# Performance work log

Measured on AMD Instinct MI355X. Metric: run time of the kernel, lower is better.

Reference implementation:

```python
import jax, jax.numpy as jnp
import numpy as np

N_NODES = 100000
N_EDGES = 3200000
D_FEAT = 256
GC_HID = 20      # CVAEEncoder.hidden_dim default
DEC_HID = 40     # CVAEDecoder.hidden_dim default
Z_DIM = 32
EXPR_DIM = 256
SIGMA_BOUND = 0.0001


def setup_inputs() -> dict:
    key = jax.random.key(0)
    ks = jax.random.split(key, 16)
    inp = {
        "nodes": jax.random.normal(ks[0], (N_NODES, D_FEAT), dtype=jnp.float32),
        "senders": jax.random.randint(ks[1], (N_EDGES,), 0, N_NODES, dtype=jnp.int32),
        "receivers": jax.random.randint(ks[2], (N_EDGES,), 0, N_NODES, dtype=jnp.int32),
        "eps": jax.random.normal(ks[3], (N_NODES, Z_DIM), dtype=jnp.float32),
    }
    def dense(k, fan_in, fan_out):
        # flax default: lecun_normal kernel, zero bias
        w = jax.random.normal(k, (fan_in, fan_out), dtype=jnp.float32) / np.sqrt(fan_in)
        return w, jnp.zeros((fan_out,), jnp.float32)
    inp["W_gc1"], inp["b_gc1"] = dense(ks[4], D_FEAT, GC_HID)
    inp["W_gc2"], inp["b_gc2"] = dense(ks[5], GC_HID, GC_HID)
    inp["W_mu"], inp["b_mu"] = dense(ks[6], GC_HID + D_FEAT, Z_DIM)
    inp["W_ls"], inp["b_ls"] = dense(ks[7], GC_HID + D_FEAT, Z_DIM)
    inp["W_d1"], inp["b_d1"] = dense(ks[8], Z_DIM, DEC_HID)
    inp["W_d2"], inp["b_d2"] = dense(ks[9], DEC_HID, EXPR_DIM)
    return inp


def _gcn_layer(h, senders, receivers, W, b):
    # jraph.GraphConvolution: update_node_fn = softmax(relu(Dense(x))),
    # then symmetric-normalized segment_sum aggregation (no self edges).
    h = jax.nn.softmax(jax.nn.relu(h @ W + b), axis=-1)  # [N, GC_HID]
    ones = jnp.ones(senders.shape, h.dtype)
    deg_s = jax.ops.segment_sum(ones, senders, N_NODES)
    deg_r = jax.ops.segment_sum(ones, receivers, N_NODES)
    h = h * jax.lax.rsqrt(jnp.maximum(deg_s, 1.0))[:, None]
    h = jax.ops.segment_sum(h[senders], receivers, N_NODES)  # irregular gather+scatter
    h = h * jax.lax.rsqrt(jnp.maximum(deg_r, 1.0))[:, None]
    return h


def reference(nodes, senders, receivers, eps,
              W_gc1, b_gc1, W_gc2, b_gc2,
              W_mu, b_mu, W_ls, b_ls,
              W_d1, b_d1, W_d2, b_d2):
    # Encoder: 2 GC layers
    h = _gcn_layer(nodes, senders, receivers, W_gc1, b_gc1)
    h = _gcn_layer(h, senders, receivers, W_gc2, b_gc2)
    h = jnp.concatenate([h, nodes], axis=-1)  # [N, GC_HID + D_FEAT]
    mu = h @ W_mu + b_mu
    logsig2 = h @ W_ls + b_ls
    # Reparameterization
    sigma = SIGMA_BOUND + jnp.exp(0.5 * logsig2)
    z = mu + sigma * eps
    # Decoder MLP (nlayers=2 -> one hidden relu layer)
    d = jax.nn.relu(z @ W_d1 + b_d1)
    Xsample = d @ W_d2 + b_d2
    return Xsample, mu, logsig2
```

## Files before the change

### kernel.cpp

```cpp
#include <hip/hip_runtime.h>
#include <math.h>

#define N_NODES 100000
#define N_EDGES 3200000
#define D_FEAT 256
#define GC_HID 20
#define DEC_HID 40
#define Z_DIM 32

#define EPB 2048
#define NBLK 1563
#define SB 392
#define SBSH 8
#define S2CAP 12288


__device__ inline unsigned short f2bf(float f) {
    unsigned u = __float_as_uint(f);
    return (unsigned short)((u + 0x7FFFu + ((u >> 16) & 1u)) >> 16);
}
__device__ inline float bf2f(unsigned short h) {
    return __uint_as_float((unsigned)h << 16);
}

__global__ __launch_bounds__(96) void k_wpack(const float* __restrict__ W1,
                                              const float* __restrict__ Wmu,
                                              const float* __restrict__ Wls,
                                              float* __restrict__ Wp) {
    int k = blockIdx.x, j = threadIdx.x;
    float v = 0.0f;
    if (j < 20) v = W1[k * GC_HID + j];
    else if (j >= 24 && j < 56) v = Wmu[(GC_HID + k) * Z_DIM + (j - 24)];
    else if (j >= 56 && j < 88) v = Wls[(GC_HID + k) * Z_DIM + (j - 56)];
    Wp[k * 96 + j] = v;
}

__global__ __launch_bounds__(512) void k_sort(const int* __restrict__ snd,
                                              const int* __restrict__ rcv,
                                              unsigned* __restrict__ rec_r,
                                              unsigned char* __restrict__ rec_s,
                                              unsigned short* __restrict__ srow_r,
                                              unsigned short* __restrict__ srow_s) {
    __shared__ int es[EPB], er[EPB];
    __shared__ unsigned scan[SB + 1];
    __shared__ unsigned cur[SB];
    __shared__ unsigned sorted[EPB];
    __shared__ unsigned char sorteds[EPB];
    int b = blockIdx.x, t = threadIdx.x;
    int base = b * EPB;
    int cnt = min(EPB, N_EDGES - base);
    for (int i = t; i < cnt; i += 512) { es[i] = snd[base + i]; er[i] = rcv[base + i]; }

    for (int i = t; i < SB + 1; i += 512) scan[i] = 0u;
    __syncthreads();
    for (int i = t; i < cnt; i += 512) atomicAdd(&scan[(er[i] >> SBSH) + 1], 1u);
    __syncthreads();
    for (int off = 1; off < SB + 1; off <<= 1) {
        unsigned v = (t >= off && t < SB + 1) ? scan[t - off] : 0u;
        __syncthreads();
        if (t < SB + 1) scan[t] += v;
        __syncthreads();
    }
    for (int i = t; i < SB + 1; i += 512) srow_r[(size_t)b * (SB + 1) + i] = (unsigned short)scan[i];
    if (t < SB) cur[t] = scan[t];
    __syncthreads();
    for (int i = t; i < cnt; i += 512) {
        int r = er[i];
        unsigned pos = atomicAdd(&cur[r >> SBSH], 1u);
        sorted[pos] = ((unsigned)(r & 255) << 17) | (unsigned)es[i];
    }
    __syncthreads();
    for (int i = t; i < cnt; i += 512) rec_r[(size_t)base + i] = sorted[i];
    __syncthreads();

    for (int i = t; i < SB + 1; i += 512) scan[i] = 0u;
    __syncthreads();
    for (int i = t; i < cnt; i += 512) atomicAdd(&scan[(es[i] >> SBSH) + 1], 1u);
    __syncthreads();
    for (int off = 1; off < SB + 1; off <<= 1) {
        unsigned v = (t >= off && t < SB + 1) ? scan[t - off] : 0u;
        __syncthreads();
        if (t < SB + 1) scan[t] += v;
        __syncthreads();
    }
    for (int i = t; i < SB + 1; i += 512) srow_s[(size_t)b * (SB + 1) + i] = (unsigned short)scan[i];
    if (t < SB) cur[t] = scan[t];
    __syncthreads();
    for (int i = t; i < cnt; i += 512) {
        int s = es[i];
        unsigned pos = atomicAdd(&cur[s >> SBSH], 1u);
        sorteds[pos] = (unsigned char)(s & 255);
    }
    __syncthreads();
    for (int i = t; i < cnt; i += 512) rec_s[(size_t)base + i] = sorteds[i];
}

__global__ __launch_bounds__(512) void k_degs(const unsigned char* __restrict__ rec_s,
                                              const unsigned short* __restrict__ srow_s,
                                              float* __restrict__ rs_s) {
    __shared__ unsigned h[256];
    int s = blockIdx.x, t = threadIdx.x;
    if (t < 256) h[t] = 0u;
    __syncthreads();
    for (int k = t; k < NBLK; k += 512) {
        const unsigned short* row = srow_s + (size_t)k * (SB + 1);
        unsigned st = row[s], en = row[s + 1];
        const unsigned char* rp = rec_s + (size_t)k * EPB;
        for (unsigned i = st; i < en; ++i) atomicAdd(&h[rp[i]], 1u);
    }
    __syncthreads();
    if (t < 256) {
        int n = (s << SBSH) + t;
        if (n < N_NODES) rs_s[n] = rsqrtf(fmaxf((float)h[t], 1.0f));
    }
}

__global__ __launch_bounds__(256) void k_scanB(const unsigned short* __restrict__ srow_r,
                                               unsigned* __restrict__ pref_t,
                                               unsigned* __restrict__ gtot) {
    __shared__ unsigned buf[256];
    int s = blockIdx.x, t = threadIdx.x;
    unsigned run = 0;
    for (int k0 = 0; k0 < NBLK; k0 += 256) {
        int k = k0 + t;
        unsigned v = 0;
        if (k < NBLK) {
            const unsigned short* row = srow_r + (size_t)k * (SB + 1);
            v = (unsigned)row[s + 1] - (unsigned)row[s];
        }
        buf[t] = v;
        __syncthreads();
        for (int off = 1; off < 256; off <<= 1) {
            unsigned x = (t >= off) ? buf[t - off] : 0u;
            __syncthreads();
            buf[t] += x;
            __syncthreads();
        }
        if (k < NBLK) pref_t[(size_t)s * NBLK + k] = run + (buf[t] - v);
        unsigned tot = buf[255];
        __syncthreads();
        run += tot;
    }
    if (t == 0) gtot[s] = run;
}

__global__ __launch_bounds__(512) void k_scanG(const unsigned* __restrict__ gtot,
                                               unsigned* __restrict__ gbase) {
    __shared__ unsigned buf[SB];
    int t = threadIdx.x;
    if (t < SB) buf[t] = gtot[t];
    __syncthreads();
    for (int off = 1; off < SB; off <<= 1) {
        unsigned x = (t >= off && t < SB) ? buf[t - off] : 0u;
        __syncthreads();
        if (t < SB) buf[t] += x;
        __syncthreads();
    }
    if (t < SB) gbase[t + 1] = buf[t];
    if (t == 0) gbase[0] = 0u;
}

__global__ __launch_bounds__(256) void k_gscat(const unsigned* __restrict__ rec_r,
                                               const unsigned short* __restrict__ srow_r,
                                               const unsigned* __restrict__ pref_t,
                                               const unsigned* __restrict__ gbase,
                                               unsigned* __restrict__ grec) {
    __shared__ unsigned recs[EPB];
    __shared__ unsigned short srow[SB + 1];
    int b = blockIdx.x, t = threadIdx.x;
    int base = b * EPB;
    int cnt = min(EPB, N_EDGES - base);
    for (int i = t; i < cnt; i += 256) recs[i] = rec_r[(size_t)base + i];
    for (int i = t; i < SB + 1; i += 256) srow[i] = srow_r[(size_t)b * (SB + 1) + i];
    __syncthreads();
    for (int s = t; s < SB; s += 256) {
        unsigned lo = srow[s], hi = srow[s + 1];
        if (lo == hi) continue;
        unsigned dst = gbase[s] + pref_t[(size_t)s * NBLK + b];
        for (unsigned i = lo; i < hi; ++i) grec[dst + (i - lo)] = recs[i];
    }
}

__global__ __launch_bounds__(256) void k_sort2(unsigned* __restrict__ grec,
                                               const unsigned* __restrict__ gbase,
                                               unsigned* __restrict__ row_ptr) {
    __shared__ unsigned recs[S2CAP];
    __shared__ unsigned hist[256];
    __shared__ unsigned scan[256];
    __shared__ unsigned cur[256];
    int s = blockIdx.x, t = threadIdx.x;
    unsigned lo = gbase[s], hi = gbase[s + 1];
    unsigned cnt = min(hi - lo, (unsigned)S2CAP);
    for (unsigned i = t; i < cnt; i += 256) recs[i] = grec[lo + i];
    hist[t] = 0u;
    __syncthreads();
    for (unsigned i = t; i < cnt; i += 256) atomicAdd(&hist[recs[i] >> 17], 1u);
    __syncthreads();
    unsigned v = hist[t];
    scan[t] = v;
    __syncthreads();
    for (int off = 1; off < 256; off <<= 1) {
        unsigned x = (t >= off) ? scan[t - off] : 0u;
        __syncthreads();
        scan[t] += x;
        __syncthreads();
    }
    unsigned excl = scan[t] - v;
    {
        int n = (s << SBSH) + t;
        if (n <= N_NODES) row_ptr[n] = lo + excl;
    }
    cur[t] = excl;
    __syncthreads();
    for (unsigned i = t; i < cnt; i += 256) {
        unsigned rec = recs[i];
        unsigned pos = atomicAdd(&cur[rec >> 17], 1u);
        grec[lo + pos] = rec & 0x1FFFFu;
    }
}

__global__ __launch_bounds__(320) void k_gather(const unsigned* __restrict__ row_ptr,
                                                const unsigned* __restrict__ grec,
                                                const float* __restrict__ src,
                                                float* __restrict__ dst) {
    int gid = blockIdx.x * 320 + threadIdx.x;
    int node = gid / 5, q = gid % 5;
    if (node >= N_NODES) return;
    unsigned lo = row_ptr[node], hi = row_ptr[node + 1];
    float4 a0 = make_float4(0.f, 0.f, 0.f, 0.f);
    float4 a1 = make_float4(0.f, 0.f, 0.f, 0.f);
    float4 a2 = make_float4(0.f, 0.f, 0.f, 0.f);
    float4 a3 = make_float4(0.f, 0.f, 0.f, 0.f);
    unsigned e = lo;
    for (; e + 4 <= hi; e += 4) {
        unsigned s0 = grec[e], s1 = grec[e + 1], s2 = grec[e + 2], s3 = grec[e + 3];
        float4 v0 = ((const float4*)src)[s0 * 5 + q];
        float4 v1 = ((const float4*)src)[s1 * 5 + q];
        float4 v2 = ((const float4*)src)[s2 * 5 + q];
        float4 v3 = ((const float4*)src)[s3 * 5 + q];
        a0.x += v0.x; a0.y += v0.y; a0.z += v0.z; a0.w += v0.w;
        a1.x += v1.x; a1.y += v1.y; a1.z += v1.z; a1.w += v1.w;
        a2.x += v2.x; a2.y += v2.y; a2.z += v2.z; a2.w += v2.w;
        a3.x += v3.x; a3.y += v3.y; a3.z += v3.z; a3.w += v3.w;
    }
    for (; e < hi; ++e) {
        unsigned s0 = grec[e];
        float4 v0 = ((const float4*)src)[s0 * 5 + q];
        a0.x += v0.x; a0.y += v0.y; a0.z += v0.z; a0.w += v0.w;
    }
    a0.x += a1.x + a2.x + a3.x;
    a0.y += a1.y + a2.y + a3.y;
    a0.z += a1.z + a2.z + a3.z;
    a0.w += a1.w + a2.w + a3.w;
    float sc = rsqrtf(fmaxf((float)(hi - lo), 1.0f));
    a0.x *= sc; a0.y *= sc; a0.z *= sc; a0.w *= sc;
    ((float4*)dst)[node * 5 + q] = a0;
}

__global__ __launch_bounds__(256) void k_gc1f(const float* __restrict__ nodes,
                                              const float* __restrict__ Wp,
                                              const float* __restrict__ b1,
                                              const float* __restrict__ rs_s,
                                              float* __restrict__ h_pre,
                                              unsigned short* __restrict__ pml) {
    __shared__ float tile[2][64 * 33];
    float* gb = &tile[0][0];
    int t = threadIdx.x;
    int g = __builtin_amdgcn_readfirstlane(t >> 6);
    int lane = t & 63;
    int n0 = blockIdx.x * 64;
    int node = n0 + lane;

    {
        int idx = t;
#pragma unroll
        for (int r = 0; r < 2; ++r, idx += 256) {
            int rr = idx >> 3, c4 = idx & 7;
            int gn = n0 + rr;
            float4 v = (gn < N_NODES)
                ? ((const float4*)nodes)[(size_t)gn * 64 + c4]
                : make_float4(0.f, 0.f, 0.f, 0.f);
            float* dst = &tile[0][rr * 33 + c4 * 4];
            dst[0] = v.x; dst[1] = v.y; dst[2] = v.z; dst[3] = v.w;
        }
    }
    __syncthreads();

    float acc[24];
#pragma unroll
    for (int j = 0; j < 24; ++j) acc[j] = 0.0f;

    for (int c = 0; c < 8; ++c) {
        float4 p0, p1;
        if (c < 7) {
            int idx = t, rr = idx >> 3, c4 = idx & 7, gn = n0 + rr;
            p0 = (gn < N_NODES)
                ? ((const float4*)nodes)[(size_t)gn * 64 + (c + 1) * 8 + c4]
                : make_float4(0.f, 0.f, 0.f, 0.f);
            idx = t + 256; rr = idx >> 3; c4 = idx & 7; gn = n0 + rr;
            p1 = (gn < N_NODES)
                ? ((const float4*)nodes)[(size_t)gn * 64 + (c + 1) * 8 + c4]
                : make_float4(0.f, 0.f, 0.f, 0.f);
        }
        const float* trow  = &tile[c & 1][lane * 33];
        const float* wbase = Wp + (size_t)(c * 32) * 96 + g * 24;
#pragma unroll 4
        for (int kk = 0; kk < 32; ++kk) {
            float x = trow[kk];
            const float* wr = wbase + kk * 96;
#pragma unroll
            for (int j = 0; j < 24; ++j) acc[j] = fmaf(x, wr[j], acc[j]);
        }
        if (c < 7) {
            int idx = t, rr = idx >> 3, c4 = idx & 7;
            float* dst = &tile[(c + 1) & 1][rr * 33 + c4 * 4];
            dst[0] = p0.x; dst[1] = p0.y; dst[2] = p0.z; dst[3] = p0.w;
            idx = t + 256; rr = idx >> 3; c4 = idx & 7;
            dst = &tile[(c + 1) & 1][rr * 33 + c4 * 4];
            dst[0] = p1.x; dst[1] = p1.y; dst[2] = p1.z; dst[3] = p1.w;
        }
        __syncthreads();
    }

    if (node < N_NODES) {
        if (g == 0) {
#pragma unroll
            for (int j = 0; j < GC_HID; ++j) gb[lane * 21 + j] = acc[j] + b1[j];
        } else {
            int base = (g - 1) * 24;
            unsigned short* pp = pml + (size_t)node * 64 + base;
            uint4 q0, q1, q2;
            q0.x = (unsigned)f2bf(acc[0]) | ((unsigned)f2bf(acc[1]) << 16);
            q0.y = (unsigned)f2bf(acc[2]) | ((unsigned)f2bf(acc[3]) << 16);
            q0.z = (unsigned)f2bf(acc[4]) | ((unsigned)f2bf(acc[5]) << 16);
            q0.w = (unsigned)f2bf(acc[6]) | ((unsigned)f2bf(acc[7]) << 16);
            q1.x = (unsigned)f2bf(acc[8]) | ((unsigned)f2bf(acc[9]) << 16);
            q1.y = (unsigned)f2bf(acc[10]) | ((unsigned)f2bf(acc[11]) << 16);
            q1.z = (unsigned)f2bf(acc[12]) | ((unsigned)f2bf(acc[13]) << 16);
            q1.w = (unsigned)f2bf(acc[14]) | ((unsigned)f2bf(acc[15]) << 16);
            q2.x = (unsigned)f2bf(acc[16]) | ((unsigned)f2bf(acc[17]) << 16);
            q2.y = (unsigned)f2bf(acc[18]) | ((unsigned)f2bf(acc[19]) << 16);
            q2.z = (unsigned)f2bf(acc[20]) | ((unsigned)f2bf(acc[21]) << 16);
            q2.w = (unsigned)f2bf(acc[22]) | ((unsigned)f2bf(acc[23]) << 16);
            ((uint4*)pp)[0] = q0;
            ((uint4*)pp)[1] = q1;
            if (g != 3) ((uint4*)pp)[2] = q2;
        }
    }
    __syncthreads();
    if (t < 64) {
        int nn = n0 + t;
        if (nn < N_NODES) {
            float v[GC_HID];
            float mx = -1e30f;
#pragma unroll
            for (int j = 0; j < GC_HID; ++j) {
                v[j] = fmaxf(gb[t * 21 + j], 0.0f);
                mx = fmaxf(mx, v[j]);
            }
            float s = 0.0f;
#pragma unroll
            for (int j = 0; j < GC_HID; ++j) {
                v[j] = __expf(v[j] - mx);
                s += v[j];
            }
            float inv = rs_s[nn] / s;
#pragma unroll
            for (int j = 0; j < GC_HID; ++j) v[j] *= inv;
            float4* o = (float4*)&h_pre[(size_t)nn * GC_HID];
            o[0] = make_float4(v[0],  v[1],  v[2],  v[3]);
            o[1] = make_float4(v[4],  v[5],  v[6],  v[7]);
            o[2] = make_float4(v[8],  v[9],  v[10], v[11]);
            o[3] = make_float4(v[12], v[13], v[14], v[15]);
            o[4] = make_float4(v[16], v[17], v[18], v[19]);
        }
    }
}

__global__ __launch_bounds__(256) void k_gc2(const float* __restrict__ h1in,
                                             const float* __restrict__ W2,
                                             const float* __restrict__ b2,
                                             const float* __restrict__ rs_s,
                                             float* __restrict__ h2_pre) {
    __shared__ float Wsh[GC_HID * GC_HID];
    __shared__ float bsh[GC_HID];
    int tid = threadIdx.x;
    if (tid < GC_HID * GC_HID) Wsh[tid] = W2[tid];
    if (tid < GC_HID) bsh[tid] = b2[tid];
    __syncthreads();
    int node = blockIdx.x * 256 + tid;
    if (node >= N_NODES) return;
    const float4* ap = (const float4*)&h1in[node * GC_HID];
    float4 a0 = ap[0], a1 = ap[1], a2 = ap[2], a3 = ap[3], a4 = ap[4];
    float h1[GC_HID] = {a0.x,a0.y,a0.z,a0.w, a1.x,a1.y,a1.z,a1.w,
                        a2.x,a2.y,a2.z,a2.w, a3.x,a3.y,a3.z,a3.w,
                        a4.x,a4.y,a4.z,a4.w};
    float t[GC_HID];
#pragma unroll
    for (int j = 0; j < GC_HID; ++j) t[j] = bsh[j];
#pragma unroll
    for (int i = 0; i < GC_HID; ++i) {
        float x = h1[i];
#pragma unroll
        for (int j = 0; j < GC_HID; ++j) t[j] = fmaf(x, Wsh[i * GC_HID + j], t[j]);
    }
    float mx = -1e30f;
#pragma unroll
    for (int j = 0; j < GC_HID; ++j) { t[j] = fmaxf(t[j], 0.0f); mx = fmaxf(mx, t[j]); }
    float s = 0.0f;
#pragma unroll
    for (int j = 0; j < GC_HID; ++j) { t[j] = __expf(t[j] - mx); s += t[j]; }
    float inv = rs_s[node] / s;
#pragma unroll
    for (int j = 0; j < GC_HID; ++j) t[j] *= inv;
    float4* o = (float4*)&h2_pre[node * GC_HID];
    o[0] = make_float4(t[0],  t[1],  t[2],  t[3]);
    o[1] = make_float4(t[4],  t[5],  t[6],  t[7]);
    o[2] = make_float4(t[8],  t[9],  t[10], t[11]);
    o[3] = make_float4(t[12], t[13], t[14], t[15]);
    o[4] = make_float4(t[16], t[17], t[18], t[19]);
}

__global__ __launch_bounds__(256) void k_enc2(const float* __restrict__ h2in,
                                              const unsigned short* __restrict__ pml,
                                              const float* __restrict__ Wmu,
                                              const float* __restrict__ bmu,
                                              const float* __restrict__ Wls,
                                              const float* __restrict__ bls,
                                              float* __restrict__ mu_out,
                                              float* __restrict__ ls_out) {
    int t = threadIdx.x;
    int wave = t >> 6, lane = t & 63;
    int og = __builtin_amdgcn_readfirstlane(wave | ((int)blockIdx.y << 2));
    int half = og >> 2;
    int co = (og & 3) << 3;
    int node = blockIdx.x * 64 + lane;
    if (node >= N_NODES) return;
    const float* W  = half ? Wls : Wmu;
    const float* bb = half ? bls : bmu;
    float* out      = half ? ls_out : mu_out;

    uint4 p = *(const uint4*)(pml + (size_t)node * 64 + half * 32 + co);
    float acc[8];
    acc[0] = bf2f((unsigned short)(p.x & 0xFFFFu));
    acc[1] = bf2f((unsigned short)(p.x >> 16));
    acc[2] = bf2f((unsigned short)(p.y & 0xFFFFu));
    acc[3] = bf2f((unsigned short)(p.y >> 16));
    acc[4] = bf2f((unsigned short)(p.z & 0xFFFFu));
    acc[5] = bf2f((unsigned short)(p.z >> 16));
    acc[6] = bf2f((unsigned short)(p.w & 0xFFFFu));
    acc[7] = bf2f((unsigned short)(p.w >> 16));
#pragma unroll
    for (int j = 0; j < 8; ++j) acc[j] += bb[co + j];

    const float4* hp = (const float4*)(h2in + (size_t)node * GC_HID);
#pragma unroll
    for (int v = 0; v < 5; ++v) {
        float4 hh = hp[v];
#pragma unroll
        for (int c = 0; c < 4; ++c) {
            float x = (c == 0) ? hh.x : (c == 1) ? hh.y : (c == 2) ? hh.z : hh.w;
            const float* wr = W + (v * 4 + c) * Z_DIM + co;
#pragma unroll
            for (int j = 0; j < 8; ++j) acc[j] = fmaf(x, wr[j], acc[j]);
        }
    }
    float4* op = (float4*)(out + (size_t)node * Z_DIM + co);
    op[0] = make_float4(acc[0], acc[1], acc[2], acc[3]);
    op[1] = make_float4(acc[4], acc[5], acc[6], acc[7]);
}

__global__ __launch_bounds__(256) void k_z(const float* __restrict__ mu,
                                           const float* __restrict__ ls,
                                           const float* __restrict__ eps,
                                           float* __restrict__ z) {
    int i = blockIdx.x * 256 + threadIdx.x;
    if (i >= N_NODES * Z_DIM / 4) return;
    float4 m = ((const float4*)mu)[i];
    float4 l = ((const float4*)ls)[i];
    float4 e = ((const float4*)eps)[i];
    float4 zz;
    zz.x = m.x + (1e-4f + __expf(0.5f * l.x)) * e.x;
    zz.y = m.y + (1e-4f + __expf(0.5f * l.y)) * e.y;
    zz.z = m.z + (1e-4f + __expf(0.5f * l.z)) * e.z;
    zz.w = m.w + (1e-4f + __expf(0.5f * l.w)) * e.w;
    ((float4*)z)[i] = zz;
}

__global__ __launch_bounds__(256) void k_decd(const float* __restrict__ z,
                                              const float* __restrict__ Wd1,
                                              const float* __restrict__ bd1,
                                              float* __restrict__ dbuf) {
    int node = blockIdx.x * 256 + threadIdx.x;
    if (node >= N_NODES) return;
    float d[DEC_HID];
#pragma unroll
    for (int j = 0; j < DEC_HID; ++j) d[j] = bd1[j];
    const float4* zp = (const float4*)(z + (size_t)node * Z_DIM);
#pragma unroll
    for (int v = 0; v < Z_DIM / 4; ++v) {
        float4 zz = zp[v];
#pragma unroll
        for (int c = 0; c < 4; ++c) {
            float x = (c == 0) ? zz.x : (c == 1) ? zz.y : (c == 2) ? zz.z : zz.w;
            const float* wr = Wd1 + (v * 4 + c) * DEC_HID;
#pragma unroll
            for (int j = 0; j < DEC_HID; ++j) d[j] = fmaf(x, wr[j], d[j]);
        }
    }
    float4* op = (float4*)(dbuf + (size_t)node * DEC_HID);
#pragma unroll
    for (int v = 0; v < DEC_HID / 4; ++v)
        op[v] = make_float4(fmaxf(d[4*v], 0.f), fmaxf(d[4*v+1], 0.f),
                            fmaxf(d[4*v+2], 0.f), fmaxf(d[4*v+3], 0.f));
}

__global__ __launch_bounds__(256) void k_decx(const float* __restrict__ dbuf,
                                              const float* __restrict__ Wd2,
                                              const float* __restrict__ bd2,
                                              float* __restrict__ X) {
    int lane = threadIdx.x & 63;
    int wv   = threadIdx.x >> 6;
    int ch   = __builtin_amdgcn_readfirstlane(((blockIdx.x & 1) << 2) | wv);
    int node = (blockIdx.x >> 1) * 64 + lane;
    if (node >= N_NODES) return;
    int co = ch << 5;
    float o[32];
#pragma unroll
    for (int j = 0; j < 32; ++j) o[j] = bd2[co + j];
    const float4* dp = (const float4*)(dbuf + (size_t)node * DEC_HID);
#pragma unroll
    for (int v = 0; v < DEC_HID / 4; ++v) {
        float4 dd = dp[v];
#pragma unroll
        for (int c = 0; c < 4; ++c) {
            float x = (c == 0) ? dd.x : (c == 1) ? dd.y : (c == 2) ? dd.z : dd.w;
            const float* wr = Wd2 + (v * 4 + c) * D_FEAT + co;
#pragma unroll
            for (int j = 0; j < 32; ++j) o[j] = fmaf(x, wr[j], o[j]);
        }
    }
    float4* xp = (float4*)(X + (size_t)node * D_FEAT + co);
#pragma unroll
    for (int v = 0; v < 8; ++v)
        xp[v] = make_float4(o[4*v], o[4*v+1], o[4*v+2], o[4*v+3]);
}

extern "C" void kernel_launch(void* const* d_in, const int* in_sizes, int n_in,
                              void* d_out, int out_size, void* d_ws, size_t ws_size,
                              hipStream_t stream) {
    const float* nodes = (const float*)d_in[0];
    const int*   snd   = (const int*)d_in[1];
    const int*   rcv   = (const int*)d_in[2];
    const float* eps   = (const float*)d_in[3];
    const float* W1    = (const float*)d_in[4];
    const float* b1    = (const float*)d_in[5];
    const float* W2    = (const float*)d_in[6];
    const float* b2    = (const float*)d_in[7];
    const float* Wmu   = (const float*)d_in[8];
    const float* bmu   = (const float*)d_in[9];
    const float* Wls   = (const float*)d_in[10];
    const float* bls   = (const float*)d_in[11];
    const float* Wd1   = (const float*)d_in[12];
    const float* bd1   = (const float*)d_in[13];
    const float* Wd2   = (const float*)d_in[14];
    const float* bd2   = (const float*)d_in[15];

    char* ws = (char*)d_ws;
    float*          h_pre    = (float*)(ws);
    float*          agg      = (float*)(ws + 8000000);
    float*          dbuf     = (float*)(ws);
    unsigned*       grec     = (unsigned*)(ws + 16000000);
    unsigned*       rec_r    = (unsigned*)(ws + 28804096);
    unsigned short* pml      = (unsigned short*)(ws + 28804096);
    unsigned short* srow_r   = (unsigned short*)(ws + 41608192);
    unsigned*       pref_t   = (unsigned*)(ws + 42836720);
    float*          zbuf     = (float*)(ws + 41608192);
    unsigned*       row_ptr  = (unsigned*)(ws + 45287504);
    unsigned*       gtot     = (unsigned*)(ws + 45687508);
    unsigned*       gbase    = (unsigned*)(ws + 45689076);
    float*          rs_s     = (float*)(ws + 45690648);
    unsigned char*  rec_s    = (unsigned char*)(ws + 46090648);
    unsigned short* srow_s   = (unsigned short*)(ws + 49291672);
    float*          Wpack    = (float*)(ws + 50520192);

    float* X      = (float*)d_out;
    float* mu_out = X + (size_t)N_NODES * D_FEAT;
    float* ls_out = mu_out + (size_t)N_NODES * Z_DIM;

    k_wpack<<<256, 96, 0, stream>>>(W1, Wmu, Wls, Wpack);
    k_sort<<<NBLK, 512, 0, stream>>>(snd, rcv, rec_r, rec_s, srow_r, srow_s);
    k_degs<<<SB, 512, 0, stream>>>(rec_s, srow_s, rs_s);
    k_scanB<<<SB, 256, 0, stream>>>(srow_r, pref_t, gtot);
    k_scanG<<<1, 512, 0, stream>>>(gtot, gbase);
    k_gscat<<<NBLK, 256, 0, stream>>>(rec_r, srow_r, pref_t, gbase, grec);
    k_sort2<<<SB, 256, 0, stream>>>(grec, gbase, row_ptr);

    k_gc1f<<<1563, 256, 0, stream>>>(nodes, Wpack, b1, rs_s, h_pre, pml);
    k_gather<<<1563, 320, 0, stream>>>(row_ptr, grec, h_pre, agg);
    k_gc2<<<391, 256, 0, stream>>>(agg, W2, b2, rs_s, h_pre);
    k_gather<<<1563, 320, 0, stream>>>(row_ptr, grec, h_pre, agg);

    k_enc2<<<dim3(1563, 2), 256, 0, stream>>>(agg, pml, Wmu, bmu, Wls, bls,
                                              mu_out, ls_out);
    k_z<<<3125, 256, 0, stream>>>(mu_out, ls_out, eps, zbuf);
    k_decd<<<391, 256, 0, stream>>>(zbuf, Wd1, bd1, dbuf);
    k_decx<<<3126, 256, 0, stream>>>(dbuf, Wd2, bd2, X);
}
```

Measured before the change: 429.5 us.

## Register-block k_gc1f GEMM as 4x8 outer product with LDS-staged weights

Rewrites the first-layer node projection kernel so each of 192 threads computes a 4-node by 8-output register tile. The node tile is stored transposed in LDS and the packed weights are double-buffered in LDS instead of being read from global memory per FMA row. The aim is to cut global and LDS traffic per FMA and raise arithmetic intensity, at the cost of more LDS use and a different thread-to-output mapping. The bias add for the softmax path moves into the epilogue.

```diff
diff --git a/kernel.cpp b/kernel.cpp
--- a/kernel.cpp
+++ b/kernel.cpp
@@ -13,6 +13,7 @@
 #define SB 392
 #define SBSH 8
 #define S2CAP 12288
+#define GF_THREADS 192
 
 
 __device__ inline unsigned short f2bf(float f) {
@@ -257,94 +258,132 @@
     ((float4*)dst)[node * 5 + q] = a0;
 }
 
-__global__ __launch_bounds__(256) void k_gc1f(const float* __restrict__ nodes,
+__global__ __launch_bounds__(192) void k_gc1f(const float* __restrict__ nodes,
                                               const float* __restrict__ Wp,
                                               const float* __restrict__ b1,
                                               const float* __restrict__ rs_s,
                                               float* __restrict__ h_pre,
                                               unsigned short* __restrict__ pml) {
-    __shared__ float tile[2][64 * 33];
-    float* gb = &tile[0][0];
+    __shared__ float xT[2][32 * 68];
+    __shared__ float wT[2][32 * 100];
     int t = threadIdx.x;
-    int g = __builtin_amdgcn_readfirstlane(t >> 6);
-    int lane = t & 63;
+    int ng = t & 15;
+    int og = t >> 4;
     int n0 = blockIdx.x * 64;
-    int node = n0 + lane;
-
-    {
-        int idx = t;
-#pragma unroll
-        for (int r = 0; r < 2; ++r, idx += 256) {
-            int rr = idx >> 3, c4 = idx & 7;
-            int gn = n0 + rr;
-            float4 v = (gn < N_NODES)
-                ? ((const float4*)nodes)[(size_t)gn * 64 + c4]
-                : make_float4(0.f, 0.f, 0.f, 0.f);
-            float* dst = &tile[0][rr * 33 + c4 * 4];
-            dst[0] = v.x; dst[1] = v.y; dst[2] = v.z; dst[3] = v.w;
-        }
-    }
-    __syncthreads();
-
-    float acc[24];
-#pragma unroll
-    for (int j = 0; j < 24; ++j) acc[j] = 0.0f;
+
+    float acc[4][8];
+#pragma unroll
+    for (int i = 0; i < 4; ++i)
+#pragma unroll
+        for (int j = 0; j < 8; ++j) acc[i][j] = 0.0f;
+
+    for (int idx = t; idx < 512; idx += GF_THREADS) {
+        int rr = idx >> 3, c4 = idx & 7;
+        int gn = n0 + rr;
+        float4 v = (gn < N_NODES)
+            ? ((const float4*)nodes)[(size_t)gn * 64 + c4]
+            : make_float4(0.f, 0.f, 0.f, 0.f);
+        xT[0][(c4 * 4 + 0) * 68 + rr] = v.x;
+        xT[0][(c4 * 4 + 1) * 68 + rr] = v.y;
+        xT[0][(c4 * 4 + 2) * 68 + rr] = v.z;
+        xT[0][(c4 * 4 + 3) * 68 + rr] = v.w;
+    }
+    for (int idx = t; idx < 768; idx += GF_THREADS) {
+        int kk = idx / 24, q = idx - kk * 24;
+        float4 v = ((const float4*)Wp)[(size_t)kk * 24 + q];
+        *(float4*)&wT[0][kk * 100 + q * 4] = v;
+    }
+    __syncthreads();
 
     for (int c = 0; c < 8; ++c) {
-        float4 p0, p1;
+        float4 px[3], pw[4];
         if (c < 7) {
-            int idx = t, rr = idx >> 3, c4 = idx & 7, gn = n0 + rr;
-            p0 = (gn < N_NODES)
-                ? ((const float4*)nodes)[(size_t)gn * 64 + (c + 1) * 8 + c4]
-                : make_float4(0.f, 0.f, 0.f, 0.f);
-            idx = t + 256; rr = idx >> 3; c4 = idx & 7; gn = n0 + rr;
-            p1 = (gn < N_NODES)
-                ? ((const float4*)nodes)[(size_t)gn * 64 + (c + 1) * 8 + c4]
-                : make_float4(0.f, 0.f, 0.f, 0.f);
-        }
-        const float* trow  = &tile[c & 1][lane * 33];
-        const float* wbase = Wp + (size_t)(c * 32) * 96 + g * 24;
+            int idx = t;
+#pragma unroll
+            for (int r = 0; r < 3; ++r, idx += GF_THREADS) {
+                if (idx < 512) {
+                    int rr = idx >> 3, c4 = idx & 7;
+                    int gn = n0 + rr;
+                    px[r] = (gn < N_NODES)
+                        ? ((const float4*)nodes)[(size_t)gn * 64 + (c + 1) * 8 + c4]
+                        : make_float4(0.f, 0.f, 0.f, 0.f);
+                }
+            }
+            idx = t;
+#pragma unroll
+            for (int r = 0; r < 4; ++r, idx += GF_THREADS) {
+                int kk = idx / 24, q = idx - kk * 24;
+                pw[r] = ((const float4*)Wp)[((size_t)(c + 1) * 32 + kk) * 24 + q];
+            }
+        }
+        const float* xb = &xT[c & 1][ng * 4];
+        const float* wb = &wT[c & 1][og * 8];
 #pragma unroll 4
         for (int kk = 0; kk < 32; ++kk) {
-            float x = trow[kk];
-            const float* wr = wbase + kk * 96;
-#pragma unroll
-            for (int j = 0; j < 24; ++j) acc[j] = fmaf(x, wr[j], acc[j]);
+            float4 xv = *(const float4*)&xb[kk * 68];
+            float4 w0 = *(const float4*)&wb[kk * 100];
+            float4 w1 = *(const float4*)&wb[kk * 100 + 4];
+            float xs0 = xv.x, xs1 = xv.y, xs2 = xv.z, xs3 = xv.w;
+            acc[0][0] = fmaf(xs0, w0.x, acc[0][0]); acc[0][1] = fmaf(xs0, w0.y, acc[0][1]);
+            acc[0][2] = fmaf(xs0, w0.z, acc[0][2]); acc[0][3] = fmaf(xs0, w0.w, acc[0][3]);
+            acc[0][4] = fmaf(xs0, w1.x, acc[0][4]); acc[0][5] = fmaf(xs0, w1.y, acc[0][5]);
+            acc[0][6] = fmaf(xs0, w1.z, acc[0][6]); acc[0][7] = fmaf(xs0, w1.w, acc[0][7]);
+            acc[1][0] = fmaf(xs1, w0.x, acc[1][0]); acc[1][1] = fmaf(xs1, w0.y, acc[1][1]);
+            acc[1][2] = fmaf(xs1, w0.z, acc[1][2]); acc[1][3] = fmaf(xs1, w0.w, acc[1][3]);
+            acc[1][4] = fmaf(xs1, w1.x, acc[1][4]); acc[1][5] = fmaf(xs1, w1.y, acc[1][5]);
+            acc[1][6] = fmaf(xs1, w1.z, acc[1][6]); acc[1][7] = fmaf(xs1, w1.w, acc[1][7]);
+            acc[2][0] = fmaf(xs2, w0.x, acc[2][0]); acc[2][1] = fmaf(xs2, w0.y, acc[2][1]);
+            acc[2][2] = fmaf(xs2, w0.z, acc[2][2]); acc[2][3] = fmaf(xs2, w0.w, acc[2][3]);
+            acc[2][4] = fmaf(xs2, w1.x, acc[2][4]); acc[2][5] = fmaf(xs2, w1.y, acc[2][5]);
+            acc[2][6] = fmaf(xs2, w1.z, acc[2][6]); acc[2][7] = fmaf(xs2, w1.w, acc[2][7]);
+            acc[3][0] = fmaf(xs3, w0.x, acc[3][0]); acc[3][1] = fmaf(xs3, w0.y, acc[3][1]);
+            acc[3][2] = fmaf(xs3, w0.z, acc[3][2]); acc[3][3] = fmaf(xs3, w0.w, acc[3][3]);
+            acc[3][4] = fmaf(xs3, w1.x, acc[3][4]); acc[3][5] = fmaf(xs3, w1.y, acc[3][5]);
+            acc[3][6] = fmaf(xs3, w1.z, acc[3][6]); acc[3][7] = fmaf(xs3, w1.w, acc[3][7]);
         }
         if (c < 7) {
-            int idx = t, rr = idx >> 3, c4 = idx & 7;
-            float* dst = &tile[(c + 1) & 1][rr * 33 + c4 * 4];
-            dst[0] = p0.x; dst[1] = p0.y; dst[2] = p0.z; dst[3] = p0.w;
-            idx = t + 256; rr = idx >> 3; c4 = idx & 7;
-            dst = &tile[(c + 1) & 1][rr * 33 + c4 * 4];
-            dst[0] = p1.x; dst[1] = p1.y; dst[2] = p1.z; dst[3] = p1.w;
-        }
-        __syncthreads();
-    }
-
-    if (node < N_NODES) {
-        if (g == 0) {
-#pragma unroll
-            for (int j = 0; j < GC_HID; ++j) gb[lane * 21 + j] = acc[j] + b1[j];
-        } else {
-            int base = (g - 1) * 24;
-            unsigned short* pp = pml + (size_t)node * 64 + base;
-            uint4 q0, q1, q2;
-            q0.x = (unsigned)f2bf(acc[0]) | ((unsigned)f2bf(acc[1]) << 16);
-            q0.y = (unsigned)f2bf(acc[2]) | ((unsigned)f2bf(acc[3]) << 16);
-            q0.z = (unsigned)f2bf(acc[4]) | ((unsigned)f2bf(acc[5]) << 16);
-            q0.w = (unsigned)f2bf(acc[6]) | ((unsigned)f2bf(acc[7]) << 16);
-            q1.x = (unsigned)f2bf(acc[8]) | ((unsigned)f2bf(acc[9]) << 16);
-            q1.y = (unsigned)f2bf(acc[10]) | ((unsigned)f2bf(acc[11]) << 16);
-            q1.z = (unsigned)f2bf(acc[12]) | ((unsigned)f2bf(acc[13]) << 16);
-            q1.w = (unsigned)f2bf(acc[14]) | ((unsigned)f2bf(acc[15]) << 16);
-            q2.x = (unsigned)f2bf(acc[16]) | ((unsigned)f2bf(acc[17]) << 16);
-            q2.y = (unsigned)f2bf(acc[18]) | ((unsigned)f2bf(acc[19]) << 16);
-            q2.z = (unsigned)f2bf(acc[20]) | ((unsigned)f2bf(acc[21]) << 16);
-            q2.w = (unsigned)f2bf(acc[22]) | ((unsigned)f2bf(acc[23]) << 16);
-            ((uint4*)pp)[0] = q0;
-            ((uint4*)pp)[1] = q1;
-            if (g != 3) ((uint4*)pp)[2] = q2;
+            int idx = t;
+#pragma unroll
+            for (int r = 0; r < 3; ++r, idx += GF_THREADS) {
+                if (idx < 512) {
+                    int rr = idx >> 3, c4 = idx & 7;
+                    float* dst = &xT[(c + 1) & 1][0];
+                    dst[(c4 * 4 + 0) * 68 + rr] = px[r].x;
+                    dst[(c4 * 4 + 1) * 68 + rr] = px[r].y;
+                    dst[(c4 * 4 + 2) * 68 + rr] = px[r].z;
+                    dst[(c4 * 4 + 3) * 68 + rr] = px[r].w;
+                }
+            }
+            idx = t;
+#pragma unroll
+            for (int r = 0; r < 4; ++r, idx += GF_THREADS) {
+                int kk = idx / 24, q = idx - kk * 24;
+                *(float4*)&wT[(c + 1) & 1][kk * 100 + q * 4] = pw[r];
+            }
+            __syncthreads();
+        }
+    }
+
+    float* gb = &xT[0][0];
+    if (og < 3) {
+#pragma unroll
+        for (int i = 0; i < 4; ++i)
+#pragma unroll
+            for (int j = 0; j < 8; ++j)
+                gb[(ng * 4 + i) * 25 + og * 8 + j] = acc[i][j];
+    } else if (og < 11) {
+        int base = og * 8 - 24;
+#pragma unroll
+        for (int i = 0; i < 4; ++i) {
+            int node = n0 + ng * 4 + i;
+            if (node < N_NODES) {
+                uint4 q;
+                q.x = (unsigned)f2bf(acc[i][0]) | ((unsigned)f2bf(acc[i][1]) << 16);
+                q.y = (unsigned)f2bf(acc[i][2]) | ((unsigned)f2bf(acc[i][3]) << 16);
+                q.z = (unsigned)f2bf(acc[i][4]) | ((unsigned)f2bf(acc[i][5]) << 16);
+                q.w = (unsigned)f2bf(acc[i][6]) | ((unsigned)f2bf(acc[i][7]) << 16);
+                *(uint4*)(pml + (size_t)node * 64 + base) = q;
+            }
         }
     }
     __syncthreads();
@@ -355,7 +394,7 @@
             float mx = -1e30f;
 #pragma unroll
             for (int j = 0; j < GC_HID; ++j) {
-                v[j] = fmaxf(gb[t * 21 + j], 0.0f);
+                v[j] = fmaxf(gb[t * 25 + j] + b1[j], 0.0f);
                 mx = fmaxf(mx, v[j]);
             }
             float s = 0.0f;
@@ -596,7 +635,7 @@
     k_gscat<<<NBLK, 256, 0, stream>>>(rec_r, srow_r, pref_t, gbase, grec);
     k_sort2<<<SB, 256, 0, stream>>>(grec, gbase, row_ptr);
 
-    k_gc1f<<<1563, 256, 0, stream>>>(nodes, Wpack, b1, rs_s, h_pre, pml);
+    k_gc1f<<<1563, GF_THREADS, 0, stream>>>(nodes, Wpack, b1, rs_s, h_pre, pml);
     k_gather<<<1563, 320, 0, stream>>>(row_ptr, grec, h_pre, agg);
     k_gc2<<<391, 256, 0, stream>>>(agg, W2, b2, rs_s, h_pre);
     k_gather<<<1563, 320, 0, stream>>>(row_ptr, grec, h_pre, agg);
```

Result: slower. 444.2 us (+3.4%).
